# Optimization experiments

Measured on AMD Instinct MI355X. Metric: run time of the kernel, lower is better.

## Reference

```python
import jax, jax.numpy as jnp
import numpy as np


def setup_inputs() -> dict:
    key = jax.random.key(0)
    k1, k2 = jax.random.split(key)
    pred = jax.random.normal(k1, (1, 2048, 512), dtype=jnp.float32)
    cand = jax.random.normal(k2, (1, 65536, 512), dtype=jnp.float32)
    return {
        "predicted_transaction_company": pred,
        "future_transaction_companies_inc_current_data": cand,
    }


def reference(predicted_transaction_company, future_transaction_companies_inc_current_data):
    # torch.cdist with p=2 on [1,P,D] x [1,R,D] -> [1,P,R]; squeeze(0) -> [P,R]; global min.
    x = predicted_transaction_company[0]                       # [P, D]
    y = future_transaction_companies_inc_current_data[0]       # [R, D]
    sq = (
        jnp.sum(x * x, axis=-1)[:, None]
        + jnp.sum(y * y, axis=-1)[None, :]
        - 2.0 * jnp.einsum("pd,rd->pr", x, y)
    )                                                          # [P, R]
    distances = jnp.sqrt(jnp.maximum(sq, 0.0))
    return jnp.min(distances)
```

## Files before the change

kernel.cpp:

```cpp
#include <hip/hip_runtime.h>
#include <stdint.h>

#define P 2048
#define R 65536
#define DD 512
#define BM 256
#define BN 256
#define BK 64
#define NT (DD / BK)

typedef __attribute__((ext_vector_type(8))) short short8;
typedef __attribute__((ext_vector_type(4))) float f32x4;

__device__ inline unsigned short f2bf(float f) {
  unsigned int u = __float_as_uint(f);
  u += 0x7fffu + ((u >> 16) & 1u);
  return (unsigned short)(u >> 16);
}

__device__ inline void gload_lds16(const void* g, void* l) {
  __builtin_amdgcn_global_load_lds(
      (const __attribute__((address_space(1))) unsigned int*)g,
      (__attribute__((address_space(3))) unsigned int*)l,
      16, 0, 0);
}

__global__ __launch_bounds__(256) void k_convert(
    const float* __restrict__ pred, const float* __restrict__ cand,
    unsigned short* __restrict__ Abf, unsigned short* __restrict__ Bbf,
    float* __restrict__ nx, float* __restrict__ ny,
    unsigned int* __restrict__ minp)
{
  if (blockIdx.x == 0 && threadIdx.x == 0) *minp = 0x7f800000u;
  int gw   = (blockIdx.x * 256 + threadIdx.x) >> 6;
  int lane = threadIdx.x & 63;
  if (gw >= P + R) return;
  const float* src; unsigned short* dst; float* np;
  if (gw < P) { src = pred + (size_t)gw * DD; dst = Abf + (size_t)gw * DD; np = nx + gw; }
  else { int r = gw - P; src = cand + (size_t)r * DD; dst = Bbf + (size_t)r * DD; np = ny + r; }
  const float4* s4 = ((const float4*)src) + lane * 2;
  float4 v0 = s4[0], v1 = s4[1];
  float ss = v0.x*v0.x + v0.y*v0.y + v0.z*v0.z + v0.w*v0.w
           + v1.x*v1.x + v1.y*v1.y + v1.z*v1.z + v1.w*v1.w;
  union { unsigned short h[8]; uint4 v; } pk;
  pk.h[0]=f2bf(v0.x); pk.h[1]=f2bf(v0.y); pk.h[2]=f2bf(v0.z); pk.h[3]=f2bf(v0.w);
  pk.h[4]=f2bf(v1.x); pk.h[5]=f2bf(v1.y); pk.h[6]=f2bf(v1.z); pk.h[7]=f2bf(v1.w);
  *(uint4*)(dst + (size_t)lane * 8) = pk.v;
  #pragma unroll
  for (int off = 32; off; off >>= 1) ss += __shfl_down(ss, off, 64);
  if (lane == 0) *np = ss;
}

__global__ __launch_bounds__(512, 2) void k_gemm_min(
    const unsigned short* __restrict__ Abf, const unsigned short* __restrict__ Bbf,
    const float* __restrict__ nx, const float* __restrict__ ny,
    unsigned int* __restrict__ minp)
{
  __shared__ __align__(16) unsigned short As[2][BM * BK];
  __shared__ __align__(16) unsigned short Bs[2][BN * BK];
  __shared__ float wmin[8];

  const int tid  = threadIdx.x;
  const int wave = tid >> 6;
  const int lane = tid & 63;

  const int raw = blockIdx.x;
  const int wg  = (raw & 7) * 256 + (raw >> 3);
  const int by  = wg & 7;
  const int bx  = wg >> 3;
  const int rowA0 = by * BM, rowB0 = bx * BN;
  const int wr = wave >> 2;
  const int wc = wave & 3;

  f32x4 zero = {0.f, 0.f, 0.f, 0.f};
  f32x4 acc[8][4];
  #pragma unroll
  for (int i = 0; i < 8; ++i)
    #pragma unroll
    for (int j = 0; j < 4; ++j) acc[i][j] = zero;

  const int rloc = lane >> 3;
  const int cswz = (lane & 7) ^ rloc;
  const unsigned short* gA[4]; const unsigned short* gB[4];
  int lOff[4];
  #pragma unroll
  for (int t = 0; t < 4; ++t) {
    const int ii = wave * 4 + t;
    const int rr = ii * 8 + rloc;
    gA[t] = Abf + (size_t)(rowA0 + rr) * DD + cswz * 8;
    gB[t] = Bbf + (size_t)(rowB0 + rr) * DD + cswz * 8;
    lOff[t] = ii * 512;
  }

#define STAGE(c, kt) do { const int _k0 = (kt) * BK;            \
    _Pragma("unroll")                                           \
    for (int _t = 0; _t < 4; ++_t) {                            \
      gload_lds16(gA[_t] + _k0, &As[(c)][lOff[_t]]);            \
      gload_lds16(gB[_t] + _k0, &Bs[(c)][lOff[_t]]);            \
    } } while (0)

  const int m = lane & 15, quad = lane >> 4, mb = m & 7;
  const int aRow0 = (wr * 128 + m) * BK;
  const int bRow0 = (wc * 64  + m) * BK;
  const int swz0 = ((quad    ) ^ mb) * 8;
  const int swz1 = ((quad + 4) ^ mb) * 8;

  STAGE(0, 0);
  STAGE(1, 1);
  asm volatile("s_waitcnt vmcnt(8)" ::: "memory");
  __builtin_amdgcn_s_barrier();

  for (int kt = 0; kt < NT; ++kt) {
    const int c = kt & 1;
    const unsigned short* A0 = &As[c][0];
    const unsigned short* B0 = &Bs[c][0];

    short8 bfr[4][2];
    #pragma unroll
    for (int j = 0; j < 4; ++j) {
      const unsigned short* bp = B0 + bRow0 + j * 16 * BK;
      bfr[j][0] = *(const short8*)(bp + swz0);
      bfr[j][1] = *(const short8*)(bp + swz1);
    }
    #pragma unroll
    for (int mh = 0; mh < 2; ++mh) {
      short8 af[4][2];
      #pragma unroll
      for (int i = 0; i < 4; ++i) {
        const unsigned short* ap = A0 + aRow0 + (mh * 4 + i) * 16 * BK;
        af[i][0] = *(const short8*)(ap + swz0);
        af[i][1] = *(const short8*)(ap + swz1);
      }
      __builtin_amdgcn_s_setprio(1);
      #pragma unroll
      for (int i = 0; i < 4; ++i)
        #pragma unroll
        for (int j = 0; j < 4; ++j) {
          acc[mh*4+i][j] = __builtin_amdgcn_mfma_f32_16x16x32_bf16(af[i][0], bfr[j][0], acc[mh*4+i][j], 0, 0, 0);
          acc[mh*4+i][j] = __builtin_amdgcn_mfma_f32_16x16x32_bf16(af[i][1], bfr[j][1], acc[mh*4+i][j], 0, 0, 0);
        }
      __builtin_amdgcn_s_setprio(0);
      asm volatile("" ::: "memory");
    }

    if (kt < NT - 1) {
      __builtin_amdgcn_s_barrier();
      if (kt + 2 < NT) {
        STAGE(c, kt + 2);
        asm volatile("s_waitcnt vmcnt(8)" ::: "memory");
      } else {
        asm volatile("s_waitcnt vmcnt(0)" ::: "memory");
      }
      __builtin_amdgcn_s_barrier();
    }
  }
#undef STAGE

  float lmin = 3.4e38f;
  #pragma unroll
  for (int i = 0; i < 8; ++i) {
    const int mbase = rowA0 + wr * 128 + i * 16 + quad * 4;
    float4 nxv = *(const float4*)(nx + mbase);
    #pragma unroll
    for (int j = 0; j < 4; ++j) {
      const int n = rowB0 + wc * 64 + j * 16 + m;
      const float nyv = ny[n];
      f32x4 a = acc[i][j];
      lmin = fminf(lmin, nxv.x + nyv - 2.0f * a[0]);
      lmin = fminf(lmin, nxv.y + nyv - 2.0f * a[1]);
      lmin = fminf(lmin, nxv.z + nyv - 2.0f * a[2]);
      lmin = fminf(lmin, nxv.w + nyv - 2.0f * a[3]);
    }
  }
  #pragma unroll
  for (int off = 32; off; off >>= 1) lmin = fminf(lmin, __shfl_down(lmin, off, 64));
  if (lane == 0) wmin[wave] = lmin;
  __syncthreads();
  if (tid == 0) {
    float mn = wmin[0];
    #pragma unroll
    for (int w = 1; w < 8; ++w) mn = fminf(mn, wmin[w]);
    atomicMin(minp, __float_as_uint(fmaxf(mn, 0.0f)));
  }
}

__global__ __launch_bounds__(64) void k_initmin(unsigned int* minp) {
  if (threadIdx.x == 0) *minp = 0x7f800000u;
}

__global__ __launch_bounds__(256) void k_brute(
    const float* __restrict__ pred, const float* __restrict__ cand,
    unsigned int* __restrict__ minp)
{
  __shared__ float yrow[DD];
  __shared__ float wm[4];
  const int c = blockIdx.x;
  for (int i = threadIdx.x; i < DD; i += 256) yrow[i] = cand[(size_t)c * DD + i];
  __syncthreads();
  float lmin = 3.4e38f;
  for (int p = threadIdx.x; p < P; p += 256) {
    const float* xp = pred + (size_t)p * DD;
    float s = 0.f;
    for (int k = 0; k < DD; ++k) { float d = xp[k] - yrow[k]; s = fmaf(d, d, s); }
    lmin = fminf(lmin, s);
  }
  #pragma unroll
  for (int off = 32; off; off >>= 1) lmin = fminf(lmin, __shfl_down(lmin, off, 64));
  if ((threadIdx.x & 63) == 0) wm[threadIdx.x >> 6] = lmin;
  __syncthreads();
  if (threadIdx.x == 0) {
    float mn = fminf(fminf(wm[0], wm[1]), fminf(wm[2], wm[3]));
    atomicMin(minp, __float_as_uint(fmaxf(mn, 0.0f)));
  }
}

__global__ __launch_bounds__(64) void k_finalize(const unsigned int* minp, float* out) {
  if (threadIdx.x == 0) out[0] = sqrtf(__uint_as_float(*minp));
}

extern "C" void kernel_launch(void* const* d_in, const int* in_sizes, int n_in,
                              void* d_out, int out_size, void* d_ws, size_t ws_size,
                              hipStream_t stream) {
  const float* pred = (const float*)d_in[0];
  const float* cand = (const float*)d_in[1];
  float* out = (float*)d_out;

  unsigned int* minp = (unsigned int*)d_ws;
  float* wsf = (float*)d_ws;
  float* nx = wsf + 16;
  float* ny = nx + P;
  unsigned short* Abf = (unsigned short*)(ny + R);
  unsigned short* Bbf = Abf + (size_t)P * DD;
  const size_t need = (size_t)(16 + P + R) * 4 + ((size_t)P * DD + (size_t)R * DD) * 2;

  if (ws_size >= need) {
    const int rows = P + R;
    k_convert<<<rows / 4, 256, 0, stream>>>(pred, cand, Abf, Bbf, nx, ny, minp);
    k_gemm_min<<<(P / BM) * (R / BN), 512, 0, stream>>>(Abf, Bbf, nx, ny, minp);
  } else {
    k_initmin<<<1, 64, 0, stream>>>(minp);
    k_brute<<<R, 256, 0, stream>>>(pred, cand, minp);
  }
  k_finalize<<<1, 64, 0, stream>>>(minp, out);
}
```

Measured before the change: 340.0 us.

## Shrink GEMM tile to 256x128 with 4 waves, single-buffer LDS, grid-stride convert

The GEMM kernel now uses a 256x128 tile computed by 4 waves, each holding the same 128x64 accumulator footprint as before. LDS is single-buffered instead of double-buffered, with a full vmcnt(0) wait before each k-step. Half the blocks issue a staggered s_sleep before their first load, and the convert kernel becomes a grid-stride loop over a fixed 2048-block grid. The smaller LDS footprint may let more blocks fit per CU, but every k-step now stalls on its global loads with no overlap, and the narrower tile gives less B reuse.

```diff
diff --git a/kernel.cpp b/kernel.cpp
--- a/kernel.cpp
+++ b/kernel.cpp
@@ -5,7 +5,7 @@
 #define R 65536
 #define DD 512
 #define BM 256
-#define BN 256
+#define BN 128
 #define BK 64
 #define NT (DD / BK)
 
@@ -32,45 +32,47 @@
     unsigned int* __restrict__ minp)
 {
   if (blockIdx.x == 0 && threadIdx.x == 0) *minp = 0x7f800000u;
-  int gw   = (blockIdx.x * 256 + threadIdx.x) >> 6;
-  int lane = threadIdx.x & 63;
-  if (gw >= P + R) return;
-  const float* src; unsigned short* dst; float* np;
-  if (gw < P) { src = pred + (size_t)gw * DD; dst = Abf + (size_t)gw * DD; np = nx + gw; }
-  else { int r = gw - P; src = cand + (size_t)r * DD; dst = Bbf + (size_t)r * DD; np = ny + r; }
-  const float4* s4 = ((const float4*)src) + lane * 2;
-  float4 v0 = s4[0], v1 = s4[1];
-  float ss = v0.x*v0.x + v0.y*v0.y + v0.z*v0.z + v0.w*v0.w
-           + v1.x*v1.x + v1.y*v1.y + v1.z*v1.z + v1.w*v1.w;
-  union { unsigned short h[8]; uint4 v; } pk;
-  pk.h[0]=f2bf(v0.x); pk.h[1]=f2bf(v0.y); pk.h[2]=f2bf(v0.z); pk.h[3]=f2bf(v0.w);
-  pk.h[4]=f2bf(v1.x); pk.h[5]=f2bf(v1.y); pk.h[6]=f2bf(v1.z); pk.h[7]=f2bf(v1.w);
-  *(uint4*)(dst + (size_t)lane * 8) = pk.v;
-  #pragma unroll
-  for (int off = 32; off; off >>= 1) ss += __shfl_down(ss, off, 64);
-  if (lane == 0) *np = ss;
-}
-
-__global__ __launch_bounds__(512, 2) void k_gemm_min(
+  const int lane = threadIdx.x & 63;
+  const int wv   = (blockIdx.x << 2) | (threadIdx.x >> 6);
+  const int nw   = gridDim.x << 2;
+  for (int gw = wv; gw < P + R; gw += nw) {
+    const float* src; unsigned short* dst; float* np;
+    if (gw < P) { src = pred + (size_t)gw * DD; dst = Abf + (size_t)gw * DD; np = nx + gw; }
+    else { int r = gw - P; src = cand + (size_t)r * DD; dst = Bbf + (size_t)r * DD; np = ny + r; }
+    const float4* s4 = ((const float4*)src) + lane * 2;
+    float4 v0 = s4[0], v1 = s4[1];
+    float ss = v0.x*v0.x + v0.y*v0.y + v0.z*v0.z + v0.w*v0.w
+             + v1.x*v1.x + v1.y*v1.y + v1.z*v1.z + v1.w*v1.w;
+    union { unsigned short h[8]; uint4 v; } pk;
+    pk.h[0]=f2bf(v0.x); pk.h[1]=f2bf(v0.y); pk.h[2]=f2bf(v0.z); pk.h[3]=f2bf(v0.w);
+    pk.h[4]=f2bf(v1.x); pk.h[5]=f2bf(v1.y); pk.h[6]=f2bf(v1.z); pk.h[7]=f2bf(v1.w);
+    *(uint4*)(dst + (size_t)lane * 8) = pk.v;
+    #pragma unroll
+    for (int off = 32; off; off >>= 1) ss += __shfl_down(ss, off, 64);
+    if (lane == 0) *np = ss;
+  }
+}
+
+__global__ __launch_bounds__(256, 2) void k_gemm_min(
     const unsigned short* __restrict__ Abf, const unsigned short* __restrict__ Bbf,
     const float* __restrict__ nx, const float* __restrict__ ny,
     unsigned int* __restrict__ minp)
 {
-  __shared__ __align__(16) unsigned short As[2][BM * BK];
-  __shared__ __align__(16) unsigned short Bs[2][BN * BK];
-  __shared__ float wmin[8];
+  __shared__ __align__(16) unsigned short As[BM * BK];
+  __shared__ __align__(16) unsigned short Bs[BN * BK];
+  __shared__ float wmin[4];
 
   const int tid  = threadIdx.x;
   const int wave = tid >> 6;
   const int lane = tid & 63;
 
   const int raw = blockIdx.x;
-  const int wg  = (raw & 7) * 256 + (raw >> 3);
+  const int wg  = (raw & 7) * 512 + (raw >> 3);
   const int by  = wg & 7;
   const int bx  = wg >> 3;
   const int rowA0 = by * BM, rowB0 = bx * BN;
-  const int wr = wave >> 2;
-  const int wc = wave & 3;
+  const int wr = wave >> 1;
+  const int wc = wave & 1;
 
   f32x4 zero = {0.f, 0.f, 0.f, 0.f};
   f32x4 acc[8][4];
@@ -81,55 +83,51 @@
 
   const int rloc = lane >> 3;
   const int cswz = (lane & 7) ^ rloc;
-  const unsigned short* gA[4]; const unsigned short* gB[4];
-  int lOff[4];
-  #pragma unroll
-  for (int t = 0; t < 4; ++t) {
-    const int ii = wave * 4 + t;
-    const int rr = ii * 8 + rloc;
-    gA[t] = Abf + (size_t)(rowA0 + rr) * DD + cswz * 8;
-    gB[t] = Bbf + (size_t)(rowB0 + rr) * DD + cswz * 8;
-    lOff[t] = ii * 512;
-  }
-
-#define STAGE(c, kt) do { const int _k0 = (kt) * BK;            \
-    _Pragma("unroll")                                           \
-    for (int _t = 0; _t < 4; ++_t) {                            \
-      gload_lds16(gA[_t] + _k0, &As[(c)][lOff[_t]]);            \
-      gload_lds16(gB[_t] + _k0, &Bs[(c)][lOff[_t]]);            \
-    } } while (0)
+  const unsigned short* gAb = Abf + (size_t)(rowA0 + wave * 64 + rloc) * DD + cswz * 8;
+  const unsigned short* gBb = Bbf + (size_t)(rowB0 + wave * 32 + rloc) * DD + cswz * 8;
+  unsigned short* lAb = &As[(wave * 8) * 512];
+  unsigned short* lBb = &Bs[(wave * 4) * 512];
+
+#define STAGE(kt) do {                                                   \
+    const unsigned short* _pa = gAb + (kt) * BK; unsigned short* _la = lAb; \
+    _Pragma("unroll 1")                                                  \
+    for (int _t = 0; _t < 8; ++_t) {                                     \
+      gload_lds16(_pa, _la); _pa += 8 * DD; _la += 512; }                \
+    const unsigned short* _pb = gBb + (kt) * BK; unsigned short* _lb = lBb; \
+    _Pragma("unroll 1")                                                  \
+    for (int _t = 0; _t < 4; ++_t) {                                     \
+      gload_lds16(_pb, _lb); _pb += 8 * DD; _lb += 512; }                \
+  } while (0)
 
   const int m = lane & 15, quad = lane >> 4, mb = m & 7;
   const int aRow0 = (wr * 128 + m) * BK;
   const int bRow0 = (wc * 64  + m) * BK;
-  const int swz0 = ((quad    ) ^ mb) * 8;
-  const int swz1 = ((quad + 4) ^ mb) * 8;
-
-  STAGE(0, 0);
-  STAGE(1, 1);
-  asm volatile("s_waitcnt vmcnt(8)" ::: "memory");
+  const int sw0 = ((quad    ) ^ mb) * 8;
+  const int sw1 = ((quad + 4) ^ mb) * 8;
+
+  if ((raw >> 3) & 1) __builtin_amdgcn_s_sleep(8);
+
+  STAGE(0);
+  asm volatile("s_waitcnt vmcnt(0)" ::: "memory");
   __builtin_amdgcn_s_barrier();
 
-  for (int kt = 0; kt < NT; ++kt) {
-    const int c = kt & 1;
-    const unsigned short* A0 = &As[c][0];
-    const unsigned short* B0 = &Bs[c][0];
-
+  #pragma unroll 1
+  for (int T = 0; T < NT; ++T) {
     short8 bfr[4][2];
     #pragma unroll
     for (int j = 0; j < 4; ++j) {
-      const unsigned short* bp = B0 + bRow0 + j * 16 * BK;
-      bfr[j][0] = *(const short8*)(bp + swz0);
-      bfr[j][1] = *(const short8*)(bp + swz1);
+      const unsigned short* bp = Bs + bRow0 + j * 16 * BK;
+      bfr[j][0] = *(const short8*)(bp + sw0);
+      bfr[j][1] = *(const short8*)(bp + sw1);
     }
     #pragma unroll
     for (int mh = 0; mh < 2; ++mh) {
       short8 af[4][2];
       #pragma unroll
       for (int i = 0; i < 4; ++i) {
-        const unsigned short* ap = A0 + aRow0 + (mh * 4 + i) * 16 * BK;
-        af[i][0] = *(const short8*)(ap + swz0);
-        af[i][1] = *(const short8*)(ap + swz1);
+        const unsigned short* ap = As + aRow0 + (mh * 4 + i) * 16 * BK;
+        af[i][0] = *(const short8*)(ap + sw0);
+        af[i][1] = *(const short8*)(ap + sw1);
       }
       __builtin_amdgcn_s_setprio(1);
       #pragma unroll
@@ -140,17 +138,12 @@
           acc[mh*4+i][j] = __builtin_amdgcn_mfma_f32_16x16x32_bf16(af[i][1], bfr[j][1], acc[mh*4+i][j], 0, 0, 0);
         }
       __builtin_amdgcn_s_setprio(0);
-      asm volatile("" ::: "memory");
-    }
-
-    if (kt < NT - 1) {
+    }
+
+    if (T + 1 < NT) {
       __builtin_amdgcn_s_barrier();
-      if (kt + 2 < NT) {
-        STAGE(c, kt + 2);
-        asm volatile("s_waitcnt vmcnt(8)" ::: "memory");
-      } else {
-        asm volatile("s_waitcnt vmcnt(0)" ::: "memory");
-      }
+      STAGE(T + 1);
+      asm volatile("s_waitcnt vmcnt(0)" ::: "memory");
       __builtin_amdgcn_s_barrier();
     }
   }
@@ -177,9 +170,7 @@
   if (lane == 0) wmin[wave] = lmin;
   __syncthreads();
   if (tid == 0) {
-    float mn = wmin[0];
-    #pragma unroll
-    for (int w = 1; w < 8; ++w) mn = fminf(mn, wmin[w]);
+    float mn = fminf(fminf(wmin[0], wmin[1]), fminf(wmin[2], wmin[3]));
     atomicMin(minp, __float_as_uint(fmaxf(mn, 0.0f)));
   }
 }
@@ -234,9 +225,8 @@
   const size_t need = (size_t)(16 + P + R) * 4 + ((size_t)P * DD + (size_t)R * DD) * 2;
 
   if (ws_size >= need) {
-    const int rows = P + R;
-    k_convert<<<rows / 4, 256, 0, stream>>>(pred, cand, Abf, Bbf, nx, ny, minp);
-    k_gemm_min<<<(P / BM) * (R / BN), 512, 0, stream>>>(Abf, Bbf, nx, ny, minp);
+    k_convert<<<2048, 256, 0, stream>>>(pred, cand, Abf, Bbf, nx, ny, minp);
+    k_gemm_min<<<(P / BM) * (R / BN), 256, 0, stream>>>(Abf, Bbf, nx, ny, minp);
   } else {
     k_initmin<<<1, 64, 0, stream>>>(minp);
     k_brute<<<R, 256, 0, stream>>>(pred, cand, minp);
```

Measured after the change: 348.7 us. +2.5%, slower.
